# Performance work log

Hardware: AMD Instinct MI355X
Metric: run time of the kernel (lower is better)

The kernel has to match this reference:

```python
import jax, jax.numpy as jnp
import numpy as np

N, D, D_QK, D_V = 8192, 1024, 128, 128

def setup_inputs() -> dict:
    key = jax.random.key(0)
    k1, k2, k3, k4 = jax.random.split(key, 4)
    s = 1.0 / np.sqrt(D)
    return {
        "x": jax.random.normal(k1, (N, D), dtype=jnp.float32),
        "Wq": jax.random.normal(k2, (D_QK, D), dtype=jnp.float32) * s,
        "Wk": jax.random.normal(k3, (D_QK, D), dtype=jnp.float32) * s,
        "Wv": jax.random.normal(k4, (D_V, D), dtype=jnp.float32) * s,
    }

def reference(x, Wq, Wk, Wv):
    # NOTE: original code MULTIPLIES by sqrt(D_qk) (dq_sqrt_inv = np.sqrt(D_qk)).
    scale = jnp.sqrt(jnp.asarray(D_QK, dtype=x.dtype))
    q = x @ Wq.T            # [N, D_qk]
    k = x @ Wk.T            # [N, D_qk]
    v = x @ Wv.T            # [N, D_v]
    scores = scale * (q @ k.T)          # [N, N]
    attn = jax.nn.softmax(scores, axis=-1)
    return attn @ v          # [N, D_v]
```

## Files before the change

kernel.cpp:

```cpp
#include <hip/hip_runtime.h>
#include <hip/hip_bf16.h>
#include <math.h>
#include <stdint.h>

#define N_TOK 8192
#define D_IN  1024
#define D_H   128
#define SPLIT 8

typedef __bf16 bf16;
typedef __attribute__((ext_vector_type(4))) __bf16 bf16x4;
typedef __attribute__((ext_vector_type(8))) __bf16 bf16x8;
typedef __attribute__((ext_vector_type(4))) float floatx4;

#define MFMA16(a, b, c) __builtin_amdgcn_mfma_f32_16x16x32_bf16((a), (b), (c), 0, 0, 0)

#define QSCALE 16.322625246404958f

__device__ __forceinline__ uint32_t pack2(float a, float b) {
    union { bf16 h[2]; uint32_t u; } z;
    z.h[0] = (bf16)a; z.h[1] = (bf16)b; return z.u;
}

__device__ __forceinline__ size_t vtf_idx(int n, int d) {
    return ((size_t)((n >> 6) * 8 + (d >> 4)) << 10)
         + (((n >> 3) & 7) << 7) + ((d & 15) << 3) + (n & 7);
}
__device__ __forceinline__ size_t khf_idx(int n, int d) {
    return ((size_t)(((n >> 6) * 4 + (d >> 5)) * 4 + ((n >> 4) & 3)) << 9)
         + (((d >> 3) & 3) << 7) + ((n & 15) << 3) + (d & 7);
}

#define X_OCT (N_TOK * D_IN / 8)
#define W_OCT (3 * D_H * D_IN / 8)

__global__ __launch_bounds__(256)
void convert_kernel(const float* __restrict__ x,
                    const float* __restrict__ Wq,
                    const float* __restrict__ Wk,
                    const float* __restrict__ Wv,
                    bf16* __restrict__ xhf, bf16* __restrict__ xlf,
                    bf16* __restrict__ whf, bf16* __restrict__ wlf)
{
    const int gid = blockIdx.x * 256 + threadIdx.x;
    const float* src;
    bf16 *dh, *dl;
    size_t doff;
    if (gid < X_OCT) {
        int lane = gid & 63, fc = gid >> 6;
        int kc = fc & 31, mt = fc >> 5;
        int n  = mt * 16 + (lane & 15);
        int k0 = kc * 32 + ((lane >> 4) << 3);
        src = x + (size_t)n * D_IN + k0;
        dh = xhf; dl = xlf; doff = (size_t)gid << 3;
    } else {
        int w = gid - X_OCT;
        int y = w >> 14, r = w & 16383;
        int lane = r & 63, fc = r >> 6;
        int kc = fc & 31, ct = fc >> 5;
        int col = ct * 16 + (lane & 15);
        int k0  = kc * 32 + ((lane >> 4) << 3);
        const float* W = (y == 0) ? Wq : (y == 1) ? Wk : Wv;
        src = W + (size_t)col * D_IN + k0;
        dh = whf; dl = wlf; doff = (size_t)w << 3;
    }
    float4 a = *(const float4*)src;
    float4 b = *(const float4*)(src + 4);
    float vv[8] = { a.x, a.y, a.z, a.w, b.x, b.y, b.z, b.w };
    bf16x8 h, l;
    #pragma unroll
    for (int j = 0; j < 8; ++j) {
        bf16 hh = (bf16)vv[j];
        h[j] = hh;
        l[j] = (bf16)(vv[j] - (float)hh);
    }
    *(bf16x8*)(dh + doff) = h;
    *(bf16x8*)(dl + doff) = l;
}

__global__ __launch_bounds__(256)
void qkv_kernel(const bf16* __restrict__ xhf, const bf16* __restrict__ xlf,
                const bf16* __restrict__ whf, const bf16* __restrict__ wlf,
                bf16* __restrict__ q_hi, bf16* __restrict__ q_lo,
                bf16* __restrict__ khf, bf16* __restrict__ klf,
                bf16* __restrict__ vtf)
{
    __shared__ bf16 w_s[2][16384];

    const int t    = threadIdx.x;
    const int lane = t & 63;
    const int wid  = t >> 6;
    const int wr   = wid >> 1;
    const int wc   = wid & 1;
    const int lid  = lane & 15;
    const int quad = lane >> 4;
    const int m0   = blockIdx.x * 64;
    const bf16* wh = whf + ((size_t)blockIdx.y << 17);
    const bf16* wl = wlf + ((size_t)blockIdx.y << 17);

    auto stage = [&](int c0, int buf) {
        #pragma unroll
        for (int i = 0; i < 8; ++i) {
            int p   = wid * 8 + i;
            int hl  = p >> 4, ct = (p >> 1) & 7, kci = p & 1;
            const bf16* src = (hl ? wl : wh)
                            + ((size_t)(ct * 32 + c0 + kci) << 9) + (lane << 3);
            bf16* dst = &w_s[buf][p << 9];
            __builtin_amdgcn_global_load_lds(
                (const __attribute__((address_space(1))) void*)src,
                (__attribute__((address_space(3))) void*)dst, 16, 0, 0);
        }
    };

    floatx4 acc[2][4];
    #pragma unroll
    for (int m = 0; m < 2; ++m)
        #pragma unroll
        for (int ct = 0; ct < 4; ++ct)
            #pragma unroll
            for (int r = 0; r < 4; ++r) acc[m][ct][r] = 0.f;

    stage(0, 0);

    for (int c = 0; c < 16; ++c) {
        const int c0 = c * 2;
        const int cb = c & 1;
        __syncthreads();
        if (c < 15) stage(c0 + 2, cb ^ 1);

        #pragma unroll
        for (int kci = 0; kci < 2; ++kci) {
            bf16x8 ah[2], al[2];
            #pragma unroll
            for (int m = 0; m < 2; ++m) {
                int mt = (m0 >> 4) + wr * 2 + m;
                const size_t xb = ((size_t)(mt * 32 + c0 + kci) << 9) + (lane << 3);
                ah[m] = *(const bf16x8*)(xhf + xb);
                al[m] = *(const bf16x8*)(xlf + xb);
            }
            #pragma unroll
            for (int ct = 0; ct < 4; ++ct) {
                const int pb = (((wc * 4 + ct) * 2 + kci) << 9) + (lane << 3);
                bf16x8 bh = *(const bf16x8*)&w_s[cb][pb];
                bf16x8 bl = *(const bf16x8*)&w_s[cb][(16 << 9) + pb];
                #pragma unroll
                for (int m = 0; m < 2; ++m) {
                    acc[m][ct] = MFMA16(ah[m], bh, acc[m][ct]);
                    acc[m][ct] = MFMA16(al[m], bh, acc[m][ct]);
                    acc[m][ct] = MFMA16(ah[m], bl, acc[m][ct]);
                }
            }
        }
    }

    if (blockIdx.y == 0) {
        #pragma unroll
        for (int s2 = 0; s2 < 2; ++s2)
            #pragma unroll
            for (int ct = 0; ct < 4; ++ct)
                #pragma unroll
                for (int r = 0; r < 4; ++r) {
                    int row = m0 + wr * 32 + s2 * 16 + quad * 4 + r;
                    int col = wc * 64 + ct * 16 + lid;
                    float a = acc[s2][ct][r] * QSCALE;
                    bf16 h = (bf16)a;
                    q_hi[(size_t)row * D_H + col] = h;
                    q_lo[(size_t)row * D_H + col] = (bf16)(a - (float)h);
                }
    } else if (blockIdx.y == 1) {
        #pragma unroll
        for (int s2 = 0; s2 < 2; ++s2)
            #pragma unroll
            for (int ct = 0; ct < 4; ++ct)
                #pragma unroll
                for (int r = 0; r < 4; ++r) {
                    int n = m0 + wr * 32 + s2 * 16 + quad * 4 + r;
                    int d = wc * 64 + ct * 16 + lid;
                    float a = acc[s2][ct][r];
                    bf16 h = (bf16)a;
                    size_t idx = khf_idx(n, d);
                    khf[idx] = h;
                    klf[idx] = (bf16)(a - (float)h);
                }
    } else {
        #pragma unroll
        for (int s2 = 0; s2 < 2; ++s2)
            #pragma unroll
            for (int ct = 0; ct < 4; ++ct)
                #pragma unroll
                for (int r = 0; r < 4; ++r) {
                    int n = m0 + wr * 32 + s2 * 16 + quad * 4 + r;
                    int d = wc * 64 + ct * 16 + lid;
                    vtf[vtf_idx(n, d)] = (bf16)acc[s2][ct][r];
                }
    }
}

#define BQ   128
#define BKEY 64

__global__ __launch_bounds__(256, 2)
void flash_kernel(const bf16* __restrict__ qh, const bf16* __restrict__ ql,
                  const bf16* __restrict__ khf, const bf16* __restrict__ klf,
                  const bf16* __restrict__ vtf,
                  bf16*  __restrict__ opart,
                  float* __restrict__ mpart,
                  float* __restrict__ lpart)
{
    __shared__ bf16 k_s[2][16384];

    const int t     = threadIdx.x;
    const int lane  = t & 63;
    const int wid   = t >> 6;
    const int lid   = lane & 15;
    const int quad  = lane >> 4;
    const int q0    = blockIdx.x * BQ;
    const int strip = wid * 32;
    const int sp    = blockIdx.y;
    const int tile0 = sp * (N_TOK / BKEY / SPLIT);
    const int tile1 = tile0 + (N_TOK / BKEY / SPLIT);

    bf16x8 b_hi[2][4], b_lo[2][4];
    #pragma unroll
    for (int ct = 0; ct < 2; ++ct) {
        const size_t rowb = (size_t)(q0 + strip + ct * 16 + lid) * D_H + quad * 8;
        #pragma unroll
        for (int kc = 0; kc < 4; ++kc) {
            b_hi[ct][kc] = *(const bf16x8*)(qh + rowb + kc * 32);
            b_lo[ct][kc] = *(const bf16x8*)(ql + rowb + kc * 32);
        }
    }

    bf16x8 vones;
    #pragma unroll
    for (int j = 0; j < 8; ++j) vones[j] = (bf16)1.0f;

    float m_run[2] = { -INFINITY, -INFINITY };
    floatx4 l_acc[2];
    #pragma unroll
    for (int ct = 0; ct < 2; ++ct)
        #pragma unroll
        for (int r = 0; r < 4; ++r) l_acc[ct][r] = 0.f;
    floatx4 o_acc[8][2];
    #pragma unroll
    for (int dt = 0; dt < 8; ++dt)
        #pragma unroll
        for (int ct = 0; ct < 2; ++ct)
            #pragma unroll
            for (int r = 0; r < 4; ++r) o_acc[dt][ct][r] = 0.f;

    auto stage = [&](int tile, int buf) {
        const bf16* gh = khf + ((size_t)tile << 13) + (wid << 11) + (lane << 3);
        const bf16* gl = klf + ((size_t)tile << 13) + (wid << 11) + (lane << 3);
        bf16* lh = &k_s[buf][wid << 11];
        bf16* ll = lh + 8192;
        #pragma unroll
        for (int i = 0; i < 4; ++i) {
            __builtin_amdgcn_global_load_lds(
                (const __attribute__((address_space(1))) void*)(gh + i * 512),
                (__attribute__((address_space(3))) void*)(lh + i * 512), 16, 0, 0);
            __builtin_amdgcn_global_load_lds(
                (const __attribute__((address_space(1))) void*)(gl + i * 512),
                (__attribute__((address_space(3))) void*)(ll + i * 512), 16, 0, 0);
        }
    };

    stage(tile0, 0);

    for (int tt = tile0; tt < tile1; ++tt) {
        const int cb = (tt - tile0) & 1;
        __syncthreads();
        if (tt + 1 < tile1) stage(tt + 1, cb ^ 1);

        const bf16* khp = &k_s[cb][0];
        const bf16* klp = &k_s[cb][8192];
        floatx4 s[4][2];
        #pragma unroll
        for (int mt = 0; mt < 4; ++mt)
            #pragma unroll
            for (int ct = 0; ct < 2; ++ct)
                #pragma unroll
                for (int r = 0; r < 4; ++r) s[mt][ct][r] = 0.f;

        #pragma unroll
        for (int kc = 0; kc < 4; ++kc)
            #pragma unroll
            for (int mt = 0; mt < 4; ++mt) {
                const int fo = ((kc * 4 + mt) << 9) + (lane << 3);
                bf16x8 ah = *(const bf16x8*)&khp[fo];
                bf16x8 al = *(const bf16x8*)&klp[fo];
                #pragma unroll
                for (int ct = 0; ct < 2; ++ct) {
                    s[mt][ct] = MFMA16(ah, b_hi[ct][kc], s[mt][ct]);
                    s[mt][ct] = MFMA16(al, b_hi[ct][kc], s[mt][ct]);
                    s[mt][ct] = MFMA16(ah, b_lo[ct][kc], s[mt][ct]);
                }
            }

        const bf16* vb = vtf + ((size_t)tt << 13) + (lane << 3);
        bf16x8 vf0[8];
        #pragma unroll
        for (int dt = 0; dt < 8; ++dt)
            vf0[dt] = *(const bf16x8*)(vb + ((size_t)dt << 10));

        float alpha[2];
        uint32_t u0[4][2], u1[4][2];
        #pragma unroll
        for (int ct = 0; ct < 2; ++ct) {
            float mx = s[0][ct][0];
            #pragma unroll
            for (int mt = 0; mt < 4; ++mt)
                #pragma unroll
                for (int r = 0; r < 4; ++r)
                    mx = fmaxf(mx, s[mt][ct][r]);
            mx = fmaxf(mx, __shfl_xor(mx, 16, 64));
            mx = fmaxf(mx, __shfl_xor(mx, 32, 64));
            float mn = fmaxf(m_run[ct], mx);
            alpha[ct] = exp2f(m_run[ct] - mn);
            m_run[ct] = mn;
            #pragma unroll
            for (int mt = 0; mt < 4; ++mt) {
                float p0 = exp2f(s[mt][ct][0] - mn);
                float p1 = exp2f(s[mt][ct][1] - mn);
                float p2 = exp2f(s[mt][ct][2] - mn);
                float p3 = exp2f(s[mt][ct][3] - mn);
                u0[mt][ct] = pack2(p0, p1);
                u1[mt][ct] = pack2(p2, p3);
            }
        }

        bf16x8 pB[2][2];
        {
            const int lsrc = ((quad & 1) << 5) + lid;
            const bool himt = (quad & 2) != 0;
            #pragma unroll
            for (int kc2 = 0; kc2 < 2; ++kc2)
                #pragma unroll
                for (int ct = 0; ct < 2; ++ct) {
                    const int mA = kc2 * 2, mB = kc2 * 2 + 1;
                    uint32_t w0a = __shfl((int)u0[mA][ct], lsrc, 64);
                    uint32_t w0b = __shfl((int)u0[mB][ct], lsrc, 64);
                    uint32_t w1a = __shfl((int)u1[mA][ct], lsrc, 64);
                    uint32_t w1b = __shfl((int)u1[mB][ct], lsrc, 64);
                    uint32_t w2a = __shfl((int)u0[mA][ct], lsrc + 16, 64);
                    uint32_t w2b = __shfl((int)u0[mB][ct], lsrc + 16, 64);
                    uint32_t w3a = __shfl((int)u1[mA][ct], lsrc + 16, 64);
                    uint32_t w3b = __shfl((int)u1[mB][ct], lsrc + 16, 64);
                    union { uint32_t w[4]; bf16x8 v; } z;
                    z.w[0] = himt ? w0b : w0a;
                    z.w[1] = himt ? w1b : w1a;
                    z.w[2] = himt ? w2b : w2a;
                    z.w[3] = himt ? w3b : w3a;
                    pB[kc2][ct] = z.v;
                }
        }

        bf16x8 vf1[8];
        #pragma unroll
        for (int dt = 0; dt < 8; ++dt)
            vf1[dt] = *(const bf16x8*)(vb + ((size_t)dt << 10) + 512);

        if (__any(alpha[0] != 1.0f || alpha[1] != 1.0f)) {
            #pragma unroll
            for (int ct = 0; ct < 2; ++ct) {
                #pragma unroll
                for (int r = 0; r < 4; ++r) l_acc[ct][r] *= alpha[ct];
                #pragma unroll
                for (int dt = 0; dt < 8; ++dt)
                    #pragma unroll
                    for (int r = 0; r < 4; ++r)
                        o_acc[dt][ct][r] *= alpha[ct];
            }
        }

        #pragma unroll
        for (int ct = 0; ct < 2; ++ct) {
            l_acc[ct] = MFMA16(vones, pB[0][ct], l_acc[ct]);
            l_acc[ct] = MFMA16(vones, pB[1][ct], l_acc[ct]);
        }
        #pragma unroll
        for (int dt = 0; dt < 8; ++dt)
            #pragma unroll
            for (int ct = 0; ct < 2; ++ct) {
                o_acc[dt][ct] = MFMA16(vf0[dt], pB[0][ct], o_acc[dt][ct]);
                o_acc[dt][ct] = MFMA16(vf1[dt], pB[1][ct], o_acc[dt][ct]);
            }
    }

    uint32_t* opw = (uint32_t*)(opart + (size_t)sp * N_TOK * D_H);
    #pragma unroll
    for (int dt = 0; dt < 8; ++dt)
        #pragma unroll
        for (int ct = 0; ct < 2; ++ct) {
            int qrow  = q0 + strip + ct * 16 + lid;
            int dbase = dt * 16 + quad * 4;
            opw[(qrow * D_H + dbase) >> 1]     = pack2(o_acc[dt][ct][0], o_acc[dt][ct][1]);
            opw[(qrow * D_H + dbase + 2) >> 1] = pack2(o_acc[dt][ct][2], o_acc[dt][ct][3]);
        }
    if (quad == 0) {
        #pragma unroll
        for (int ct = 0; ct < 2; ++ct) {
            int row = q0 + strip + ct * 16 + lid;
            mpart[(size_t)sp * N_TOK + row] = m_run[ct];
            lpart[(size_t)sp * N_TOK + row] = l_acc[ct][0];
        }
    }
}

__global__ __launch_bounds__(256)
void combine_kernel(const bf16* __restrict__ opart,
                    const float* __restrict__ mpart,
                    const float* __restrict__ lpart,
                    float* __restrict__ out)
{
    const int t   = threadIdx.x;
    const int row = blockIdx.x * 16 + (t >> 4);
    const int c0  = (t & 15) * 8;

    float ms[SPLIT], ls[SPLIT];
    float mstar = -INFINITY;
    #pragma unroll
    for (int s = 0; s < SPLIT; ++s) {
        ms[s] = mpart[(size_t)s * N_TOK + row];
        ls[s] = lpart[(size_t)s * N_TOK + row];
        mstar = fmaxf(mstar, ms[s]);
    }
    float acc[8] = {};
    float L = 0.f;
    #pragma unroll
    for (int s = 0; s < SPLIT; ++s) {
        float w = exp2f(ms[s] - mstar);
        L += w * ls[s];
        bf16x8 o = *(const bf16x8*)&opart[((size_t)s * N_TOK + row) * D_H + c0];
        #pragma unroll
        for (int j = 0; j < 8; ++j)
            acc[j] += w * (float)o[j];
    }
    float inv = 1.f / L;
    float* dst = &out[(size_t)row * D_H + c0];
    *(float4*)(dst + 0) = make_float4(acc[0] * inv, acc[1] * inv,
                                      acc[2] * inv, acc[3] * inv);
    *(float4*)(dst + 4) = make_float4(acc[4] * inv, acc[5] * inv,
                                      acc[6] * inv, acc[7] * inv);
}

extern "C" void kernel_launch(void* const* d_in, const int* in_sizes, int n_in,
                              void* d_out, int out_size, void* d_ws, size_t ws_size,
                              hipStream_t stream) {
    const float* x  = (const float*)d_in[0];
    const float* Wq = (const float*)d_in[1];
    const float* Wk = (const float*)d_in[2];
    const float* Wv = (const float*)d_in[3];
    float* out = (float*)d_out;

    bf16* wsb = (bf16*)d_ws;
    const size_t SZ = (size_t)N_TOK * D_H;
    bf16* xhf = wsb;
    bf16* xlf = xhf + (size_t)X_OCT * 8;
    bf16* whf = xlf + (size_t)X_OCT * 8;
    bf16* wlf = whf + (size_t)W_OCT * 8;
    bf16* qh  = wlf + (size_t)W_OCT * 8;
    bf16* ql  = qh + SZ;
    bf16* khf = ql + SZ;
    bf16* klf = khf + SZ;
    bf16* vtf = klf + SZ;
    bf16* opart = vtf + SZ;
    float* mpart = (float*)(opart + (size_t)SPLIT * SZ);
    float* lpart = mpart + (size_t)SPLIT * N_TOK;

    convert_kernel<<<dim3((X_OCT + W_OCT) / 256), 256, 0, stream>>>(
        x, Wq, Wk, Wv, xhf, xlf, whf, wlf);
    qkv_kernel<<<dim3(N_TOK / 64, 3), 256, 0, stream>>>(
        xhf, xlf, whf, wlf, qh, ql, khf, klf, vtf);
    flash_kernel<<<dim3(N_TOK / BQ, SPLIT), 256, 0, stream>>>(
        qh, ql, khf, klf, vtf, opart, mpart, lpart);
    combine_kernel<<<dim3(N_TOK / 16), 256, 0, stream>>>(opart, mpart, lpart, out);
}
```

Before: 191.0 us.

## Use 8 waves of 16 query rows each in flash kernel, lazy rescaling

The flash kernel now runs 512 threads per block, with each wave owning 16 query rows instead of 32. This halves the per-wave accumulator and Q-fragment registers and targets higher occupancy. Rescaling of the running max is deferred until the new max exceeds the old by a threshold, so most tiles skip the o_acc rescale. V fragments are loaded in double-buffered groups interleaved with the PV MFMAs to cut live registers. In exchange, each K tile read from LDS is now shared by fewer query rows per wave, which raises LDS traffic per FLOP, and lazy rescaling risks bf16 overflow if scores grow within the threshold.

```diff
diff --git a/kernel.cpp b/kernel.cpp
--- a/kernel.cpp
+++ b/kernel.cpp
@@ -16,6 +16,8 @@
 #define MFMA16(a, b, c) __builtin_amdgcn_mfma_f32_16x16x32_bf16((a), (b), (c), 0, 0, 0)
 
 #define QSCALE 16.322625246404958f
+
+#define RESCALE_THR 8.0f
 
 __device__ __forceinline__ uint32_t pack2(float a, float b) {
     union { bf16 h[2]; uint32_t u; } z;
@@ -199,7 +201,7 @@
 #define BQ   128
 #define BKEY 64
 
-__global__ __launch_bounds__(256, 2)
+__global__ __launch_bounds__(512, 4)
 void flash_kernel(const bf16* __restrict__ qh, const bf16* __restrict__ ql,
                   const bf16* __restrict__ khf, const bf16* __restrict__ klf,
                   const bf16* __restrict__ vtf,
@@ -215,19 +217,18 @@
     const int lid   = lane & 15;
     const int quad  = lane >> 4;
     const int q0    = blockIdx.x * BQ;
-    const int strip = wid * 32;
+    const int row   = q0 + wid * 16 + lid;
     const int sp    = blockIdx.y;
     const int tile0 = sp * (N_TOK / BKEY / SPLIT);
     const int tile1 = tile0 + (N_TOK / BKEY / SPLIT);
 
-    bf16x8 b_hi[2][4], b_lo[2][4];
-    #pragma unroll
-    for (int ct = 0; ct < 2; ++ct) {
-        const size_t rowb = (size_t)(q0 + strip + ct * 16 + lid) * D_H + quad * 8;
+    bf16x8 b_hi[4], b_lo[4];
+    {
+        const size_t rowb = (size_t)row * D_H + quad * 8;
         #pragma unroll
         for (int kc = 0; kc < 4; ++kc) {
-            b_hi[ct][kc] = *(const bf16x8*)(qh + rowb + kc * 32);
-            b_lo[ct][kc] = *(const bf16x8*)(ql + rowb + kc * 32);
+            b_hi[kc] = *(const bf16x8*)(qh + rowb + kc * 32);
+            b_lo[kc] = *(const bf16x8*)(ql + rowb + kc * 32);
         }
     }
 
@@ -235,27 +236,23 @@
     #pragma unroll
     for (int j = 0; j < 8; ++j) vones[j] = (bf16)1.0f;
 
-    float m_run[2] = { -INFINITY, -INFINITY };
-    floatx4 l_acc[2];
-    #pragma unroll
-    for (int ct = 0; ct < 2; ++ct)
-        #pragma unroll
-        for (int r = 0; r < 4; ++r) l_acc[ct][r] = 0.f;
-    floatx4 o_acc[8][2];
+    float m_run = -INFINITY;
+    floatx4 l_acc;
+    #pragma unroll
+    for (int r = 0; r < 4; ++r) l_acc[r] = 0.f;
+    floatx4 o_acc[8];
     #pragma unroll
     for (int dt = 0; dt < 8; ++dt)
         #pragma unroll
-        for (int ct = 0; ct < 2; ++ct)
-            #pragma unroll
-            for (int r = 0; r < 4; ++r) o_acc[dt][ct][r] = 0.f;
+        for (int r = 0; r < 4; ++r) o_acc[dt][r] = 0.f;
 
     auto stage = [&](int tile, int buf) {
-        const bf16* gh = khf + ((size_t)tile << 13) + (wid << 11) + (lane << 3);
-        const bf16* gl = klf + ((size_t)tile << 13) + (wid << 11) + (lane << 3);
-        bf16* lh = &k_s[buf][wid << 11];
+        const bf16* gh = khf + ((size_t)tile << 13) + (wid << 10) + (lane << 3);
+        const bf16* gl = klf + ((size_t)tile << 13) + (wid << 10) + (lane << 3);
+        bf16* lh = &k_s[buf][wid << 10];
         bf16* ll = lh + 8192;
         #pragma unroll
-        for (int i = 0; i < 4; ++i) {
+        for (int i = 0; i < 2; ++i) {
             __builtin_amdgcn_global_load_lds(
                 (const __attribute__((address_space(1))) void*)(gh + i * 512),
                 (__attribute__((address_space(3))) void*)(lh + i * 512), 16, 0, 0);
@@ -274,13 +271,11 @@
 
         const bf16* khp = &k_s[cb][0];
         const bf16* klp = &k_s[cb][8192];
-        floatx4 s[4][2];
+        floatx4 s[4];
         #pragma unroll
         for (int mt = 0; mt < 4; ++mt)
             #pragma unroll
-            for (int ct = 0; ct < 2; ++ct)
-                #pragma unroll
-                for (int r = 0; r < 4; ++r) s[mt][ct][r] = 0.f;
+            for (int r = 0; r < 4; ++r) s[mt][r] = 0.f;
 
         #pragma unroll
         for (int kc = 0; kc < 4; ++kc)
@@ -289,121 +284,112 @@
                 const int fo = ((kc * 4 + mt) << 9) + (lane << 3);
                 bf16x8 ah = *(const bf16x8*)&khp[fo];
                 bf16x8 al = *(const bf16x8*)&klp[fo];
-                #pragma unroll
-                for (int ct = 0; ct < 2; ++ct) {
-                    s[mt][ct] = MFMA16(ah, b_hi[ct][kc], s[mt][ct]);
-                    s[mt][ct] = MFMA16(al, b_hi[ct][kc], s[mt][ct]);
-                    s[mt][ct] = MFMA16(ah, b_lo[ct][kc], s[mt][ct]);
-                }
+                s[mt] = MFMA16(ah, b_hi[kc], s[mt]);
+                s[mt] = MFMA16(al, b_hi[kc], s[mt]);
+                s[mt] = MFMA16(ah, b_lo[kc], s[mt]);
             }
 
         const bf16* vb = vtf + ((size_t)tt << 13) + (lane << 3);
-        bf16x8 vf0[8];
-        #pragma unroll
-        for (int dt = 0; dt < 8; ++dt)
-            vf0[dt] = *(const bf16x8*)(vb + ((size_t)dt << 10));
-
-        float alpha[2];
-        uint32_t u0[4][2], u1[4][2];
-        #pragma unroll
-        for (int ct = 0; ct < 2; ++ct) {
-            float mx = s[0][ct][0];
-            #pragma unroll
-            for (int mt = 0; mt < 4; ++mt)
-                #pragma unroll
-                for (int r = 0; r < 4; ++r)
-                    mx = fmaxf(mx, s[mt][ct][r]);
-            mx = fmaxf(mx, __shfl_xor(mx, 16, 64));
-            mx = fmaxf(mx, __shfl_xor(mx, 32, 64));
-            float mn = fmaxf(m_run[ct], mx);
-            alpha[ct] = exp2f(m_run[ct] - mn);
-            m_run[ct] = mn;
-            #pragma unroll
-            for (int mt = 0; mt < 4; ++mt) {
-                float p0 = exp2f(s[mt][ct][0] - mn);
-                float p1 = exp2f(s[mt][ct][1] - mn);
-                float p2 = exp2f(s[mt][ct][2] - mn);
-                float p3 = exp2f(s[mt][ct][3] - mn);
-                u0[mt][ct] = pack2(p0, p1);
-                u1[mt][ct] = pack2(p2, p3);
-            }
-        }
-
-        bf16x8 pB[2][2];
+        bf16x8 vf[2][4];
+        #pragma unroll
+        for (int d2 = 0; d2 < 2; ++d2)
+            #pragma unroll
+            for (int kc2 = 0; kc2 < 2; ++kc2)
+                vf[0][d2 * 2 + kc2] =
+                    *(const bf16x8*)(vb + (d2 << 10) + (kc2 << 9));
+
+        float mx = s[0][0];
+        #pragma unroll
+        for (int mt = 0; mt < 4; ++mt)
+            #pragma unroll
+            for (int r = 0; r < 4; ++r)
+                mx = fmaxf(mx, s[mt][r]);
+        mx = fmaxf(mx, __shfl_xor(mx, 16, 64));
+        mx = fmaxf(mx, __shfl_xor(mx, 32, 64));
+
+        const bool need = __any(mx - m_run > RESCALE_THR);
+        const float m_old = m_run;
+        if (need) m_run = fmaxf(m_run, mx);
+
+        uint32_t u0[4], u1[4];
+        #pragma unroll
+        for (int mt = 0; mt < 4; ++mt) {
+            float p0 = exp2f(s[mt][0] - m_run);
+            float p1 = exp2f(s[mt][1] - m_run);
+            float p2 = exp2f(s[mt][2] - m_run);
+            float p3 = exp2f(s[mt][3] - m_run);
+            u0[mt] = pack2(p0, p1);
+            u1[mt] = pack2(p2, p3);
+        }
+
+        bf16x8 pB[2];
         {
             const int lsrc = ((quad & 1) << 5) + lid;
             const bool himt = (quad & 2) != 0;
             #pragma unroll
-            for (int kc2 = 0; kc2 < 2; ++kc2)
-                #pragma unroll
-                for (int ct = 0; ct < 2; ++ct) {
-                    const int mA = kc2 * 2, mB = kc2 * 2 + 1;
-                    uint32_t w0a = __shfl((int)u0[mA][ct], lsrc, 64);
-                    uint32_t w0b = __shfl((int)u0[mB][ct], lsrc, 64);
-                    uint32_t w1a = __shfl((int)u1[mA][ct], lsrc, 64);
-                    uint32_t w1b = __shfl((int)u1[mB][ct], lsrc, 64);
-                    uint32_t w2a = __shfl((int)u0[mA][ct], lsrc + 16, 64);
-                    uint32_t w2b = __shfl((int)u0[mB][ct], lsrc + 16, 64);
-                    uint32_t w3a = __shfl((int)u1[mA][ct], lsrc + 16, 64);
-                    uint32_t w3b = __shfl((int)u1[mB][ct], lsrc + 16, 64);
-                    union { uint32_t w[4]; bf16x8 v; } z;
-                    z.w[0] = himt ? w0b : w0a;
-                    z.w[1] = himt ? w1b : w1a;
-                    z.w[2] = himt ? w2b : w2a;
-                    z.w[3] = himt ? w3b : w3a;
-                    pB[kc2][ct] = z.v;
-                }
-        }
-
-        bf16x8 vf1[8];
-        #pragma unroll
-        for (int dt = 0; dt < 8; ++dt)
-            vf1[dt] = *(const bf16x8*)(vb + ((size_t)dt << 10) + 512);
-
-        if (__any(alpha[0] != 1.0f || alpha[1] != 1.0f)) {
-            #pragma unroll
-            for (int ct = 0; ct < 2; ++ct) {
-                #pragma unroll
-                for (int r = 0; r < 4; ++r) l_acc[ct][r] *= alpha[ct];
-                #pragma unroll
-                for (int dt = 0; dt < 8; ++dt)
+            for (int kc2 = 0; kc2 < 2; ++kc2) {
+                const int mA = kc2 * 2, mB = kc2 * 2 + 1;
+                uint32_t w0a = __shfl((int)u0[mA], lsrc, 64);
+                uint32_t w0b = __shfl((int)u0[mB], lsrc, 64);
+                uint32_t w1a = __shfl((int)u1[mA], lsrc, 64);
+                uint32_t w1b = __shfl((int)u1[mB], lsrc, 64);
+                uint32_t w2a = __shfl((int)u0[mA], lsrc + 16, 64);
+                uint32_t w2b = __shfl((int)u0[mB], lsrc + 16, 64);
+                uint32_t w3a = __shfl((int)u1[mA], lsrc + 16, 64);
+                uint32_t w3b = __shfl((int)u1[mB], lsrc + 16, 64);
+                union { uint32_t w[4]; bf16x8 v; } z;
+                z.w[0] = himt ? w0b : w0a;
+                z.w[1] = himt ? w1b : w1a;
+                z.w[2] = himt ? w2b : w2a;
+                z.w[3] = himt ? w3b : w3a;
+                pB[kc2] = z.v;
+            }
+        }
+
+        if (need) {
+            const float alpha = exp2f(m_old - m_run);
+            #pragma unroll
+            for (int r = 0; r < 4; ++r) l_acc[r] *= alpha;
+            #pragma unroll
+            for (int dt = 0; dt < 8; ++dt)
+                #pragma unroll
+                for (int r = 0; r < 4; ++r)
+                    o_acc[dt][r] *= alpha;
+        }
+
+        l_acc = MFMA16(vones, pB[0], l_acc);
+        l_acc = MFMA16(vones, pB[1], l_acc);
+
+        #pragma unroll
+        for (int g = 0; g < 4; ++g) {
+            if (g < 3) {
+                #pragma unroll
+                for (int d2 = 0; d2 < 2; ++d2)
                     #pragma unroll
-                    for (int r = 0; r < 4; ++r)
-                        o_acc[dt][ct][r] *= alpha[ct];
-            }
-        }
-
-        #pragma unroll
-        for (int ct = 0; ct < 2; ++ct) {
-            l_acc[ct] = MFMA16(vones, pB[0][ct], l_acc[ct]);
-            l_acc[ct] = MFMA16(vones, pB[1][ct], l_acc[ct]);
-        }
-        #pragma unroll
-        for (int dt = 0; dt < 8; ++dt)
-            #pragma unroll
-            for (int ct = 0; ct < 2; ++ct) {
-                o_acc[dt][ct] = MFMA16(vf0[dt], pB[0][ct], o_acc[dt][ct]);
-                o_acc[dt][ct] = MFMA16(vf1[dt], pB[1][ct], o_acc[dt][ct]);
-            }
+                    for (int kc2 = 0; kc2 < 2; ++kc2)
+                        vf[(g + 1) & 1][d2 * 2 + kc2] =
+                            *(const bf16x8*)(vb + (((g + 1) * 2 + d2) << 10)
+                                                + (kc2 << 9));
+            }
+            #pragma unroll
+            for (int d2 = 0; d2 < 2; ++d2) {
+                const int dt = g * 2 + d2;
+                o_acc[dt] = MFMA16(vf[g & 1][d2 * 2 + 0], pB[0], o_acc[dt]);
+                o_acc[dt] = MFMA16(vf[g & 1][d2 * 2 + 1], pB[1], o_acc[dt]);
+            }
+        }
     }
 
     uint32_t* opw = (uint32_t*)(opart + (size_t)sp * N_TOK * D_H);
     #pragma unroll
-    for (int dt = 0; dt < 8; ++dt)
-        #pragma unroll
-        for (int ct = 0; ct < 2; ++ct) {
-            int qrow  = q0 + strip + ct * 16 + lid;
-            int dbase = dt * 16 + quad * 4;
-            opw[(qrow * D_H + dbase) >> 1]     = pack2(o_acc[dt][ct][0], o_acc[dt][ct][1]);
-            opw[(qrow * D_H + dbase + 2) >> 1] = pack2(o_acc[dt][ct][2], o_acc[dt][ct][3]);
-        }
+    for (int dt = 0; dt < 8; ++dt) {
+        int dbase = dt * 16 + quad * 4;
+        opw[(row * D_H + dbase) >> 1]     = pack2(o_acc[dt][0], o_acc[dt][1]);
+        opw[(row * D_H + dbase + 2) >> 1] = pack2(o_acc[dt][2], o_acc[dt][3]);
+    }
     if (quad == 0) {
-        #pragma unroll
-        for (int ct = 0; ct < 2; ++ct) {
-            int row = q0 + strip + ct * 16 + lid;
-            mpart[(size_t)sp * N_TOK + row] = m_run[ct];
-            lpart[(size_t)sp * N_TOK + row] = l_acc[ct][0];
-        }
+        mpart[(size_t)sp * N_TOK + row] = m_run;
+        lpart[(size_t)sp * N_TOK + row] = l_acc[0];
     }
 }
 
@@ -472,7 +458,7 @@
         x, Wq, Wk, Wv, xhf, xlf, whf, wlf);
     qkv_kernel<<<dim3(N_TOK / 64, 3), 256, 0, stream>>>(
         xhf, xlf, whf, wlf, qh, ql, khf, klf, vtf);
-    flash_kernel<<<dim3(N_TOK / BQ, SPLIT), 256, 0, stream>>>(
+    flash_kernel<<<dim3(N_TOK / BQ, SPLIT), 512, 0, stream>>>(
         qh, ql, khf, klf, vtf, opart, mpart, lpart);
     combine_kernel<<<dim3(N_TOK / 16), 256, 0, stream>>>(opart, mpart, lpart, out);
 }
```

New measurement: 195.7 us. +2.5%, slower.

## Software-pipeline QK^T across tiles, add lazy rescale threshold, stream V loads

Applied to the files above, without the earlier changes.

The attention loop is restructured so the QK^T scores for the next K tile are computed before the softmax/PV work of the current tile, using two score register sets and two LDS buffers. This overlaps matrix work with the exp and shuffle work. The running max is now updated only when a tile's max exceeds it by more than a threshold, which skips most accumulator rescales. V fragment loads are split into smaller staged chunks interleaved with the PV MFMAs to cut register pressure. The loop assumes an even number of tiles per split, and the lazy max allows exp values up to 2^8, which could affect bf16 precision.

```diff
diff --git a/kernel.cpp b/kernel.cpp
--- a/kernel.cpp
+++ b/kernel.cpp
@@ -16,6 +16,8 @@
 #define MFMA16(a, b, c) __builtin_amdgcn_mfma_f32_16x16x32_bf16((a), (b), (c), 0, 0, 0)
 
 #define QSCALE 16.322625246404958f
+
+#define RESCALE_THR 8.0f
 
 __device__ __forceinline__ uint32_t pack2(float a, float b) {
     union { bf16 h[2]; uint32_t u; } z;
@@ -265,23 +267,15 @@
         }
     };
 
-    stage(tile0, 0);
-
-    for (int tt = tile0; tt < tile1; ++tt) {
-        const int cb = (tt - tile0) & 1;
-        __syncthreads();
-        if (tt + 1 < tile1) stage(tt + 1, cb ^ 1);
-
+    auto computeS = [&](int cb, floatx4 (&s)[4][2], float (&mx)[2]) {
         const bf16* khp = &k_s[cb][0];
         const bf16* klp = &k_s[cb][8192];
-        floatx4 s[4][2];
         #pragma unroll
         for (int mt = 0; mt < 4; ++mt)
             #pragma unroll
             for (int ct = 0; ct < 2; ++ct)
                 #pragma unroll
                 for (int r = 0; r < 4; ++r) s[mt][ct][r] = 0.f;
-
         #pragma unroll
         for (int kc = 0; kc < 4; ++kc)
             #pragma unroll
@@ -296,38 +290,59 @@
                     s[mt][ct] = MFMA16(ah, b_lo[ct][kc], s[mt][ct]);
                 }
             }
-
+        #pragma unroll
+        for (int ct = 0; ct < 2; ++ct) {
+            float a0 = fmaxf(s[0][ct][0], s[0][ct][1]);
+            float a1 = fmaxf(s[0][ct][2], s[0][ct][3]);
+            float a2 = fmaxf(s[1][ct][0], s[1][ct][1]);
+            float a3 = fmaxf(s[1][ct][2], s[1][ct][3]);
+            float a4 = fmaxf(s[2][ct][0], s[2][ct][1]);
+            float a5 = fmaxf(s[2][ct][2], s[2][ct][3]);
+            float a6 = fmaxf(s[3][ct][0], s[3][ct][1]);
+            float a7 = fmaxf(s[3][ct][2], s[3][ct][3]);
+            float b0 = fmaxf(a0, a1), b1 = fmaxf(a2, a3);
+            float b2 = fmaxf(a4, a5), b3 = fmaxf(a6, a7);
+            float c0 = fmaxf(fmaxf(b0, b1), fmaxf(b2, b3));
+            c0 = fmaxf(c0, __shfl_xor(c0, 16, 64));
+            c0 = fmaxf(c0, __shfl_xor(c0, 32, 64));
+            mx[ct] = c0;
+        }
+    };
+
+    auto finish = [&](int tt, floatx4 (&s)[4][2], float (&mx)[2]) {
         const bf16* vb = vtf + ((size_t)tt << 13) + (lane << 3);
-        bf16x8 vf0[8];
-        #pragma unroll
-        for (int dt = 0; dt < 8; ++dt)
-            vf0[dt] = *(const bf16x8*)(vb + ((size_t)dt << 10));
-
-        float alpha[2];
+
+        const bool need = __any((mx[0] - m_run[0] > RESCALE_THR) ||
+                                (mx[1] - m_run[1] > RESCALE_THR));
+        float alpha[2] = { 1.f, 1.f };
+        if (need) {
+            #pragma unroll
+            for (int ct = 0; ct < 2; ++ct) {
+                float mn = fmaxf(m_run[ct], mx[ct]);
+                alpha[ct] = exp2f(m_run[ct] - mn);
+                m_run[ct] = mn;
+            }
+        }
+
         uint32_t u0[4][2], u1[4][2];
         #pragma unroll
-        for (int ct = 0; ct < 2; ++ct) {
-            float mx = s[0][ct][0];
-            #pragma unroll
-            for (int mt = 0; mt < 4; ++mt)
-                #pragma unroll
-                for (int r = 0; r < 4; ++r)
-                    mx = fmaxf(mx, s[mt][ct][r]);
-            mx = fmaxf(mx, __shfl_xor(mx, 16, 64));
-            mx = fmaxf(mx, __shfl_xor(mx, 32, 64));
-            float mn = fmaxf(m_run[ct], mx);
-            alpha[ct] = exp2f(m_run[ct] - mn);
-            m_run[ct] = mn;
+        for (int ct = 0; ct < 2; ++ct)
             #pragma unroll
             for (int mt = 0; mt < 4; ++mt) {
-                float p0 = exp2f(s[mt][ct][0] - mn);
-                float p1 = exp2f(s[mt][ct][1] - mn);
-                float p2 = exp2f(s[mt][ct][2] - mn);
-                float p3 = exp2f(s[mt][ct][3] - mn);
+                float p0 = exp2f(s[mt][ct][0] - m_run[ct]);
+                float p1 = exp2f(s[mt][ct][1] - m_run[ct]);
+                float p2 = exp2f(s[mt][ct][2] - m_run[ct]);
+                float p3 = exp2f(s[mt][ct][3] - m_run[ct]);
                 u0[mt][ct] = pack2(p0, p1);
                 u1[mt][ct] = pack2(p2, p3);
             }
-        }
+
+        bf16x8 vA[2][2];
+        #pragma unroll
+        for (int d2 = 0; d2 < 2; ++d2)
+            #pragma unroll
+            for (int kc2 = 0; kc2 < 2; ++kc2)
+                vA[d2][kc2] = *(const bf16x8*)(vb + (d2 << 10) + (kc2 << 9));
 
         bf16x8 pB[2][2];
         {
@@ -355,12 +370,7 @@
                 }
         }
 
-        bf16x8 vf1[8];
-        #pragma unroll
-        for (int dt = 0; dt < 8; ++dt)
-            vf1[dt] = *(const bf16x8*)(vb + ((size_t)dt << 10) + 512);
-
-        if (__any(alpha[0] != 1.0f || alpha[1] != 1.0f)) {
+        if (need) {
             #pragma unroll
             for (int ct = 0; ct < 2; ++ct) {
                 #pragma unroll
@@ -378,13 +388,70 @@
             l_acc[ct] = MFMA16(vones, pB[0][ct], l_acc[ct]);
             l_acc[ct] = MFMA16(vones, pB[1][ct], l_acc[ct]);
         }
-        #pragma unroll
-        for (int dt = 0; dt < 8; ++dt)
+
+        bf16x8 vB[2][2];
+        #pragma unroll
+        for (int d2 = 0; d2 < 2; ++d2)
+            #pragma unroll
+            for (int kc2 = 0; kc2 < 2; ++kc2)
+                vB[d2][kc2] = *(const bf16x8*)(vb + ((2 + d2) << 10) + (kc2 << 9));
+        #pragma unroll
+        for (int d2 = 0; d2 < 2; ++d2)
             #pragma unroll
             for (int ct = 0; ct < 2; ++ct) {
-                o_acc[dt][ct] = MFMA16(vf0[dt], pB[0][ct], o_acc[dt][ct]);
-                o_acc[dt][ct] = MFMA16(vf1[dt], pB[1][ct], o_acc[dt][ct]);
-            }
+                o_acc[d2][ct] = MFMA16(vA[d2][0], pB[0][ct], o_acc[d2][ct]);
+                o_acc[d2][ct] = MFMA16(vA[d2][1], pB[1][ct], o_acc[d2][ct]);
+            }
+        #pragma unroll
+        for (int d2 = 0; d2 < 2; ++d2)
+            #pragma unroll
+            for (int kc2 = 0; kc2 < 2; ++kc2)
+                vA[d2][kc2] = *(const bf16x8*)(vb + ((4 + d2) << 10) + (kc2 << 9));
+        #pragma unroll
+        for (int d2 = 0; d2 < 2; ++d2)
+            #pragma unroll
+            for (int ct = 0; ct < 2; ++ct) {
+                o_acc[2 + d2][ct] = MFMA16(vB[d2][0], pB[0][ct], o_acc[2 + d2][ct]);
+                o_acc[2 + d2][ct] = MFMA16(vB[d2][1], pB[1][ct], o_acc[2 + d2][ct]);
+            }
+        #pragma unroll
+        for (int d2 = 0; d2 < 2; ++d2)
+            #pragma unroll
+            for (int kc2 = 0; kc2 < 2; ++kc2)
+                vB[d2][kc2] = *(const bf16x8*)(vb + ((6 + d2) << 10) + (kc2 << 9));
+        #pragma unroll
+        for (int d2 = 0; d2 < 2; ++d2)
+            #pragma unroll
+            for (int ct = 0; ct < 2; ++ct) {
+                o_acc[4 + d2][ct] = MFMA16(vA[d2][0], pB[0][ct], o_acc[4 + d2][ct]);
+                o_acc[4 + d2][ct] = MFMA16(vA[d2][1], pB[1][ct], o_acc[4 + d2][ct]);
+            }
+        #pragma unroll
+        for (int d2 = 0; d2 < 2; ++d2)
+            #pragma unroll
+            for (int ct = 0; ct < 2; ++ct) {
+                o_acc[6 + d2][ct] = MFMA16(vB[d2][0], pB[0][ct], o_acc[6 + d2][ct]);
+                o_acc[6 + d2][ct] = MFMA16(vB[d2][1], pB[1][ct], o_acc[6 + d2][ct]);
+            }
+    };
+
+    floatx4 sA[4][2], sB[4][2];
+    float mxA[2], mxB[2];
+
+    stage(tile0, 0);
+    __syncthreads();
+    stage(tile0 + 1, 1);
+    computeS(0, sA, mxA);
+
+    for (int tt = tile0; tt < tile1; tt += 2) {
+        __syncthreads();
+        if (tt + 2 < tile1) stage(tt + 2, 0);
+        computeS(1, sB, mxB);
+        finish(tt, sA, mxA);
+        __syncthreads();
+        if (tt + 3 < tile1) stage(tt + 3, 1);
+        if (tt + 2 < tile1) computeS(0, sA, mxA);
+        finish(tt + 1, sB, mxB);
     }
 
     uint32_t* opw = (uint32_t*)(opart + (size_t)sp * N_TOK * D_H);
```

Result: slower. 219.6 us (+15.0%).
